# Kernel tuning notes

Measured on AMD Instinct MI355X. Metric: run time of the kernel, lower is better.

The kernel has to match this reference:

```python
import jax, jax.numpy as jnp
import numpy as np

# Dims (see shape_source)
B, C_IN, H, W = 32, 256, 56, 56
O, J = 256, 64            # out_channels, in_connects (sparse in-channel subset per out channel)
KH, KW = 3, 3
STRIDE = (1, 1)
PAD = (1, 1)


def setup_inputs() -> dict:
    key = jax.random.key(0)
    k1, k2 = jax.random.split(key)
    x = jax.random.normal(k1, (B, C_IN, H, W), dtype=jnp.float32)
    # init_rand_indices: each out channel samples in_connects distinct in-channels
    rng = np.random.default_rng(0)
    w_idx = jnp.asarray(
        np.stack([rng.permutation(C_IN)[:J] for _ in range(O)]), dtype=jnp.int32
    )  # [O, J]
    # reset_parameters: uniform(-stdv, +stdv), stdv = 1/sqrt(in_connects * kh * kw)
    stdv = 1.0 / np.sqrt(J * KH * KW)
    w_vals = jax.random.uniform(k2, (O, J, KH, KW), dtype=jnp.float32,
                                minval=-stdv, maxval=stdv)
    return {"x": x, "w_vals": w_vals, "w_idx": w_idx}


def reference(x, w_vals, w_idx):
    # Sparse conv: out[b,o] = sum_j conv(x[:, w_idx[o,j]], w_vals[o,j]).
    # Equivalent math: scatter sparse weights into a dense [O, C_in, KH, KW]
    # kernel (zeros on unselected channels) and run one dense conv.
    dense_w = jnp.zeros((O, C_IN, KH, KW), dtype=w_vals.dtype)
    dense_w = dense_w.at[jnp.arange(O)[:, None], w_idx].set(w_vals)
    out = jax.lax.conv_general_dilated(
        x, dense_w,
        window_strides=STRIDE,
        padding=[(PAD[0], PAD[0]), (PAD[1], PAD[1])],
        dimension_numbers=("NCHW", "OIHW", "NCHW"),
    )  # [B, O, H, W]
    return out
```

## Files before the change

kernel.cpp:

```cpp
#include <hip/hip_runtime.h>
#include <hip/hip_bf16.h>


typedef __attribute__((ext_vector_type(8))) short bf16x8;
typedef __attribute__((ext_vector_type(4))) float f32x4;

#define WD_BYTES 1179648
#define XP_BYTES 55115776
#define WS_NEED  (WD_BYTES + XP_BYTES)
#define ABUF  16384
#define BHOFF 32768
#define LDS_TOT 77824

__global__ __launch_bounds__(256) void preproc(
    const float* __restrict__ x, const float* __restrict__ wv,
    const int* __restrict__ widx, __hip_bfloat16* __restrict__ wd,
    __hip_bfloat16* __restrict__ xp)
{
    int bid = blockIdx.x;
    int tid = threadIdx.x;
    if (bid >= 1792) {
        int o = bid - 1792;
        int j = tid & 63;
        if (tid < 64) {
#pragma unroll
            for (int k = 0; k < 9; ++k)
                reinterpret_cast<float2*>(wd + (size_t)k * 65536 + o * 256)[j] =
                    float2{0.f, 0.f};
        }
        __syncthreads();
        if (tid < 64) {
            int cin = widx[o * 64 + j];
            const float* src = wv + (size_t)(o * 64 + j) * 9;
#pragma unroll
            for (int k = 0; k < 9; ++k)
                wd[(size_t)k * 65536 + o * 256 + cin] = __float2bfloat16(src[k]);
        }
        return;
    }
    int b = bid / 56, h = bid - (bid / 56) * 56;
    __shared__ __hip_bfloat16 tile[56][264];
    int c = tid;
    const float* src = x + ((size_t)(b * 256 + c)) * 3136 + h * 56;
    float vals[56];
#pragma unroll
    for (int i = 0; i < 14; ++i) {
        float4 v = *reinterpret_cast<const float4*>(src + i * 4);
        vals[i*4+0] = v.x; vals[i*4+1] = v.y; vals[i*4+2] = v.z; vals[i*4+3] = v.w;
    }
#pragma unroll
    for (int w = 0; w < 56; ++w) tile[w][c] = __float2bfloat16(vals[w]);

    char* rowb = (char*)xp + (((size_t)b * 58 + (h + 1)) * 58) * 512;
    if (tid < 64)        reinterpret_cast<double*>(rowb)[tid] = 0.0;
    else if (tid < 128)  *reinterpret_cast<double*>(rowb + 57 * 512 + (tid - 64) * 8) = 0.0;
    if (h == 0) {
        char* r0 = (char*)xp + (((size_t)b * 58 + 0) * 58) * 512;
        for (int i = tid; i < 58 * 64; i += 256) reinterpret_cast<double*>(r0)[i] = 0.0;
    }
    if (h == 55) {
        char* r57 = (char*)xp + (((size_t)b * 58 + 57) * 58) * 512;
        for (int i = tid; i < 58 * 64; i += 256) reinterpret_cast<double*>(r57)[i] = 0.0;
    }

    __syncthreads();
    char* obase = (char*)xp + (((size_t)b * 58 + (h + 1)) * 58) * 512;
#pragma unroll
    for (int k = 0; k < 7; ++k) {
        int i = tid + k * 256;
        int w = i >> 5, cc = i & 31;
        bf16x8 v = *reinterpret_cast<const bf16x8*>(&tile[w][cc * 8]);
        *reinterpret_cast<bf16x8*>(obase + (size_t)(w + 1) * 512 + cc * 16) = v;
    }
}


__device__ __forceinline__ void gload_lds16(const void* g, void* l) {
    __builtin_amdgcn_global_load_lds(
        (const __attribute__((address_space(1))) void*)g,
        (__attribute__((address_space(3))) void*)l, 16, 0, 0);
}

__device__ __forceinline__ void stage_a4(const char* wdB, char* smem, int dstA,
                                         int wid, int sa_off, int aoff) {
#pragma unroll
    for (int J = 0; J < 4; ++J)
        gload_lds16(wdB + aoff + J * 16384 + sa_off,
                    smem + dstA + (J * 32 + wid * 8) * 128);
}

__device__ __forceinline__ void stage_bh11(const char* xpOcs, char* smem,
                                           int wid, int lane) {
#pragma unroll
    for (int j = 0; j < 11; ++j) {
        int beta = j * 4096 + wid * 1024 + lane * 16;
        int rb = beta >> 7;
        int c  = (beta >> 4) & 7;
        int src = (rb < 348) ? (rb * 512 + ((c ^ (rb & 7)) << 4)) : 0;
        gload_lds16(xpOcs + src, smem + BHOFF + j * 4096 + wid * 1024);
    }
}

#define BAR() __builtin_amdgcn_s_barrier()
#define VMCNT0() asm volatile("s_waitcnt vmcnt(0)" ::: "memory")

__global__ __launch_bounds__(256, 2) void sparse_conv_mfma2b(
    const __hip_bfloat16* __restrict__ wd, const __hip_bfloat16* __restrict__ xp,
    float* __restrict__ out)
{
    extern __shared__ char smem[];
    const char* wdB = (const char*)wd;
    const char* xpB = (const char*)xp;

    const int bid = blockIdx.x;
    const int swz = (bid & 7) * 112 + (bid >> 3);
    const int mt = swz & 1;
    const int nt = swz >> 1;

    const int t = threadIdx.x;
    const int lane = t & 63, wid = t >> 6;
    const int wr = wid >> 1, wc = wid & 1;

    const int axor = (((lane & 7) ^ (lane >> 3)) * 16);
    const int sa_off = (wid * 8 + (lane >> 3)) * 512 + axor;
    const int mtOff = mt * 65536;

    const int a_rb = (lane & 15) * 128;
    const int xq0 = (((lane >> 4)) ^ (lane & 7)) * 16;
    const int xq1 = ((4 + (lane >> 4)) ^ (lane & 7)) * 16;
    const int wrOff = wr * 8192;

    const int p0 = nt * 224;
    const int bImg = p0 / 3136;
    const int r0 = (p0 - bImg * 3136) / 56;
    const char* xpO = xpB + (size_t)((bImg * 58 + r0) * 58) * 512;

    int rowpl[7];
#pragma unroll
    for (int n = 0; n < 7; ++n) {
        int q = wc * 112 + n * 16 + (lane & 15);
        int qr = q / 56;
        rowpl[n] = qr * 58 + (q - qr * 56);
    }
    const int g4 = lane >> 4;

    f32x4 acc[4][7] = {};

    stage_bh11(xpO, smem, wid, lane);
    stage_a4(wdB, smem, 0, wid, sa_off, mtOff);
    VMCNT0();
    BAR();

    int k9 = 0, cs = 0, shift = 0;
    for (int g = 0; g < 36; ++g) {
        int k9n = k9 + 1, csn = cs;
        if (k9n == 9) { k9n = 0; csn = cs + 1; if (csn == 4) csn = 0; }
        stage_a4(wdB, smem, ((g + 1) & 1) * ABUF, wid, sa_off,
                 k9n * 131072 + mtOff + csn * 128);

        const int abase = (g & 1) * ABUF + wrOff + a_rb;
        bf16x8 af0[4], af1[4], bf0[7], bf1[7];
#pragma unroll
        for (int mi = 0; mi < 4; ++mi) {
            af0[mi] = *(const bf16x8*)(smem + abase + mi * 2048 + xq0);
            af1[mi] = *(const bf16x8*)(smem + abase + mi * 2048 + xq1);
        }
#pragma unroll
        for (int n = 0; n < 7; ++n) {
            int roff = rowpl[n] + shift;
            int ba = BHOFF + (roff << 7) + ((g4 ^ (roff & 7)) << 4);
            bf0[n] = *(const bf16x8*)(smem + ba);
            bf1[n] = *(const bf16x8*)(smem + (ba ^ 64));
        }

        __builtin_amdgcn_s_setprio(1);
#pragma unroll
        for (int mi = 0; mi < 4; ++mi)
#pragma unroll
            for (int ni = 0; ni < 7; ++ni)
                acc[mi][ni] = __builtin_amdgcn_mfma_f32_16x16x32_bf16(
                    af0[mi], bf0[ni], acc[mi][ni], 0, 0, 0);
#pragma unroll
        for (int mi = 0; mi < 4; ++mi)
#pragma unroll
            for (int ni = 0; ni < 7; ++ni)
                acc[mi][ni] = __builtin_amdgcn_mfma_f32_16x16x32_bf16(
                    af1[mi], bf1[ni], acc[mi][ni], 0, 0, 0);
        __builtin_amdgcn_s_setprio(0);

        VMCNT0();
        BAR();

        if (k9n == 0) {
            if (csn != 0) {
                stage_bh11(xpO + csn * 128, smem, wid, lane);
                VMCNT0();
                BAR();
            }
            shift = 0;
        } else {
            shift += ((k9n % 3) == 0) ? 56 : 1;
        }
        k9 = k9n; cs = csn;
    }

#pragma unroll
    for (int n = 0; n < 7; ++n) {
        int p = nt * 224 + wc * 112 + n * 16;
        int pb = p / 3136;
        int rem0 = p - pb * 3136;
#pragma unroll
        for (int m = 0; m < 4; ++m) {
            int o = mt * 128 + wr * 64 + m * 16 + (lane >> 4) * 4;
            float* dst = out + ((size_t)(pb * 256 + o)) * 3136 + rem0 + (lane & 15);
#pragma unroll
            for (int r = 0; r < 4; ++r) dst[(size_t)r * 3136] = acc[m][n][r];
        }
    }
}


__global__ __launch_bounds__(256) void sparse_conv_direct(
    const float* __restrict__ x, const float* __restrict__ wv,
    const int* __restrict__ widx, float* __restrict__ out)
{
    const int bid = blockIdx.x;
    const int b = bid >> 8, o = bid & 255;
    const int tid = threadIdx.x;
    __shared__ float plane[58 * 60];
    const int rt = tid >> 3, ct = tid & 7;
    const int r0 = rt * 2, c0 = ct * 7;
    const bool active = (rt < 28);
    float acc[2][7];
#pragma unroll
    for (int i = 0; i < 2; ++i)
#pragma unroll
        for (int c = 0; c < 7; ++c) acc[i][c] = 0.f;
    const float* xb = x + (size_t)b * 256 * 3136;
    const int* idxp = widx + o * 64;
    const float* wp0 = wv + (size_t)o * 64 * 9;
    for (int j = 0; j < 64; ++j) {
        const int cin = idxp[j];
        const float* src = xb + cin * 3136;
        __syncthreads();
        for (int i = tid; i < 58 * 58; i += 256) {
            const int r = i / 58, c = i - r * 58;
            const int h = r - 1, w = c - 1;
            float v = 0.f;
            if ((unsigned)h < 56u && (unsigned)w < 56u) v = src[h * 56 + w];
            plane[r * 60 + c] = v;
        }
        float wreg[9];
#pragma unroll
        for (int k = 0; k < 9; ++k) wreg[k] = wp0[j * 9 + k];
        __syncthreads();
        if (active) {
            float rows[4][9];
#pragma unroll
            for (int dr = 0; dr < 4; ++dr)
#pragma unroll
                for (int cc = 0; cc < 9; ++cc)
                    rows[dr][cc] = plane[(r0 + dr) * 60 + (c0 + cc)];
#pragma unroll
            for (int i = 0; i < 2; ++i)
#pragma unroll
                for (int cc = 0; cc < 7; ++cc) {
                    float s = acc[i][cc];
#pragma unroll
                    for (int kh = 0; kh < 3; ++kh)
#pragma unroll
                        for (int kw = 0; kw < 3; ++kw)
                            s += rows[i + kh][cc + kw] * wreg[kh * 3 + kw];
                    acc[i][cc] = s;
                }
        }
    }
    if (active) {
        float* op = out + (size_t)bid * 3136;
#pragma unroll
        for (int i = 0; i < 2; ++i)
#pragma unroll
            for (int cc = 0; cc < 7; ++cc)
                op[(r0 + i) * 56 + (c0 + cc)] = acc[i][cc];
    }
}

extern "C" void kernel_launch(void* const* d_in, const int* in_sizes, int n_in,
                              void* d_out, int out_size, void* d_ws, size_t ws_size,
                              hipStream_t stream) {
    const float* x    = (const float*)d_in[0];
    const float* wv   = (const float*)d_in[1];
    const int*   widx = (const int*)d_in[2];
    float* out = (float*)d_out;
    (void)in_sizes; (void)n_in; (void)out_size;

    if (ws_size < (size_t)WS_NEED) {
        sparse_conv_direct<<<dim3(32 * 256), dim3(256), 0, stream>>>(x, wv, widx, out);
        return;
    }

    __hip_bfloat16* wd = (__hip_bfloat16*)d_ws;
    __hip_bfloat16* xp = (__hip_bfloat16*)((char*)d_ws + WD_BYTES);

    preproc<<<dim3(32 * 56 + 256), dim3(256), 0, stream>>>(x, wv, widx, wd, xp);

    (void)hipFuncSetAttribute((const void*)sparse_conv_mfma2b,
                              hipFuncAttributeMaxDynamicSharedMemorySize, LDS_TOT);
    sparse_conv_mfma2b<<<dim3(896), dim3(256), LDS_TOT, stream>>>(wd, xp, out);
}
```

Before: 125.4 us.

## Pre-swizzle weights into MFMA fragment layout and load A directly from global

The preprocessing kernel now writes the densified bf16 weights in a layout matching the MFMA A-fragment order, so each lane reads its fragment with a single 16-byte global load. The conv kernel drops LDS staging and double-buffering of weights, which removes the per-iteration barrier and vmcnt wait and cuts LDS use, possibly allowing more blocks per CU. Zeroing of the weight buffer moves to a hipMemsetAsync. The cost is that weight fragment loads become global/L2 latency on the critical path right before the MFMAs, with no software prefetch.

New measurement: 138.0 us. +10.1%, slower.

```diff
diff --git a/kernel.cpp b/kernel.cpp
--- a/kernel.cpp
+++ b/kernel.cpp
@@ -8,33 +8,29 @@
 #define WD_BYTES 1179648
 #define XP_BYTES 55115776
 #define WS_NEED  (WD_BYTES + XP_BYTES)
-#define ABUF  16384
-#define BHOFF 32768
-#define LDS_TOT 77824
+#define LDS_TOT  45056
 
 __global__ __launch_bounds__(256) void preproc(
     const float* __restrict__ x, const float* __restrict__ wv,
-    const int* __restrict__ widx, __hip_bfloat16* __restrict__ wd,
+    const int* __restrict__ widx, __hip_bfloat16* __restrict__ wd2,
     __hip_bfloat16* __restrict__ xp)
 {
     int bid = blockIdx.x;
     int tid = threadIdx.x;
     if (bid >= 1792) {
         int o = bid - 1792;
-        int j = tid & 63;
         if (tid < 64) {
-#pragma unroll
-            for (int k = 0; k < 9; ++k)
-                reinterpret_cast<float2*>(wd + (size_t)k * 65536 + o * 256)[j] =
-                    float2{0.f, 0.f};
-        }
-        __syncthreads();
-        if (tid < 64) {
+            int j = tid;
             int cin = widx[o * 64 + j];
             const float* src = wv + (size_t)(o * 64 + j) * 9;
+            int mt = o >> 7, wr = (o >> 6) & 1, mi = (o >> 4) & 3, lr = o & 15;
+            int cs = cin >> 6, c6 = cin & 63;
+            int s = c6 >> 5, g = (c6 >> 3) & 3, b = cin & 7;
+            size_t e0 = (size_t)(cs * 2 + mt) * 8192 + wr * 4096 +
+                        (mi * 2 + s) * 512 + (g * 16 + lr) * 8 + b;
 #pragma unroll
             for (int k = 0; k < 9; ++k)
-                wd[(size_t)k * 65536 + o * 256 + cin] = __float2bfloat16(src[k]);
+                wd2[e0 + (size_t)k * 65536] = __float2bfloat16(src[k]);
         }
         return;
     }
@@ -81,14 +77,6 @@
         (__attribute__((address_space(3))) void*)l, 16, 0, 0);
 }
 
-__device__ __forceinline__ void stage_a4(const char* wdB, char* smem, int dstA,
-                                         int wid, int sa_off, int aoff) {
-#pragma unroll
-    for (int J = 0; J < 4; ++J)
-        gload_lds16(wdB + aoff + J * 16384 + sa_off,
-                    smem + dstA + (J * 32 + wid * 8) * 128);
-}
-
 __device__ __forceinline__ void stage_bh11(const char* xpOcs, char* smem,
                                            int wid, int lane) {
 #pragma unroll
@@ -97,19 +85,19 @@
         int rb = beta >> 7;
         int c  = (beta >> 4) & 7;
         int src = (rb < 348) ? (rb * 512 + ((c ^ (rb & 7)) << 4)) : 0;
-        gload_lds16(xpOcs + src, smem + BHOFF + j * 4096 + wid * 1024);
+        gload_lds16(xpOcs + src, smem + j * 4096 + wid * 1024);
     }
 }
 
 #define BAR() __builtin_amdgcn_s_barrier()
 #define VMCNT0() asm volatile("s_waitcnt vmcnt(0)" ::: "memory")
 
-__global__ __launch_bounds__(256, 2) void sparse_conv_mfma2b(
-    const __hip_bfloat16* __restrict__ wd, const __hip_bfloat16* __restrict__ xp,
+__global__ __launch_bounds__(256, 2) void sparse_conv_afrag(
+    const __hip_bfloat16* __restrict__ wd2, const __hip_bfloat16* __restrict__ xp,
     float* __restrict__ out)
 {
     extern __shared__ char smem[];
-    const char* wdB = (const char*)wd;
+    const char* wd2B = (const char*)wd2;
     const char* xpB = (const char*)xp;
 
     const int bid = blockIdx.x;
@@ -121,14 +109,7 @@
     const int lane = t & 63, wid = t >> 6;
     const int wr = wid >> 1, wc = wid & 1;
 
-    const int axor = (((lane & 7) ^ (lane >> 3)) * 16);
-    const int sa_off = (wid * 8 + (lane >> 3)) * 512 + axor;
-    const int mtOff = mt * 65536;
-
-    const int a_rb = (lane & 15) * 128;
-    const int xq0 = (((lane >> 4)) ^ (lane & 7)) * 16;
-    const int xq1 = ((4 + (lane >> 4)) ^ (lane & 7)) * 16;
-    const int wrOff = wr * 8192;
+    const char* pA0 = wd2B + mt * 16384 + wr * 8192 + lane * 16;
 
     const int p0 = nt * 224;
     const int bImg = p0 / 3136;
@@ -147,28 +128,22 @@
     f32x4 acc[4][7] = {};
 
     stage_bh11(xpO, smem, wid, lane);
-    stage_a4(wdB, smem, 0, wid, sa_off, mtOff);
     VMCNT0();
     BAR();
 
     int k9 = 0, cs = 0, shift = 0;
     for (int g = 0; g < 36; ++g) {
-        int k9n = k9 + 1, csn = cs;
-        if (k9n == 9) { k9n = 0; csn = cs + 1; if (csn == 4) csn = 0; }
-        stage_a4(wdB, smem, ((g + 1) & 1) * ABUF, wid, sa_off,
-                 k9n * 131072 + mtOff + csn * 128);
-
-        const int abase = (g & 1) * ABUF + wrOff + a_rb;
+        const char* pA = pA0 + k9 * 131072 + cs * 32768;
         bf16x8 af0[4], af1[4], bf0[7], bf1[7];
 #pragma unroll
         for (int mi = 0; mi < 4; ++mi) {
-            af0[mi] = *(const bf16x8*)(smem + abase + mi * 2048 + xq0);
-            af1[mi] = *(const bf16x8*)(smem + abase + mi * 2048 + xq1);
+            af0[mi] = *(const bf16x8*)(pA + mi * 2048);
+            af1[mi] = *(const bf16x8*)(pA + mi * 2048 + 1024);
         }
 #pragma unroll
         for (int n = 0; n < 7; ++n) {
             int roff = rowpl[n] + shift;
-            int ba = BHOFF + (roff << 7) + ((g4 ^ (roff & 7)) << 4);
+            int ba = (roff << 7) + ((g4 ^ (roff & 7)) << 4);
             bf0[n] = *(const bf16x8*)(smem + ba);
             bf1[n] = *(const bf16x8*)(smem + (ba ^ 64));
         }
@@ -188,11 +163,11 @@
                     af1[mi], bf1[ni], acc[mi][ni], 0, 0, 0);
         __builtin_amdgcn_s_setprio(0);
 
-        VMCNT0();
-        BAR();
-
+        int k9n = k9 + 1, csn = cs;
+        if (k9n == 9) { k9n = 0; csn = cs + 1; if (csn == 4) csn = 0; }
         if (k9n == 0) {
             if (csn != 0) {
+                BAR();
                 stage_bh11(xpO + csn * 128, smem, wid, lane);
                 VMCNT0();
                 BAR();
@@ -299,12 +274,13 @@
         return;
     }
 
-    __hip_bfloat16* wd = (__hip_bfloat16*)d_ws;
-    __hip_bfloat16* xp = (__hip_bfloat16*)((char*)d_ws + WD_BYTES);
-
-    preproc<<<dim3(32 * 56 + 256), dim3(256), 0, stream>>>(x, wv, widx, wd, xp);
-
-    (void)hipFuncSetAttribute((const void*)sparse_conv_mfma2b,
+    __hip_bfloat16* wd2 = (__hip_bfloat16*)d_ws;
+    __hip_bfloat16* xp  = (__hip_bfloat16*)((char*)d_ws + WD_BYTES);
+
+    hipMemsetAsync(wd2, 0, WD_BYTES, stream);
+    preproc<<<dim3(32 * 56 + 256), dim3(256), 0, stream>>>(x, wv, widx, wd2, xp);
+
+    (void)hipFuncSetAttribute((const void*)sparse_conv_afrag,
                               hipFuncAttributeMaxDynamicSharedMemorySize, LDS_TOT);
-    sparse_conv_mfma2b<<<dim3(896), dim3(256), LDS_TOT, stream>>>(wd, xp, out);
-}
+    sparse_conv_afrag<<<dim3(896), dim3(256), LDS_TOT, stream>>>(wd2, xp, out);
+}
```
